# Optimization experiments

Hardware: AMD Instinct MI355X
Metric: run time of the kernel (lower is better)

## Reference

```python
import math
import jax, jax.numpy as jnp
import numpy as np

NUM_HEADS = 16
N_WIRES = 8  # d_k, fixed by the quantum circuit
EMBED_DIM = NUM_HEADS * N_WIRES  # 128
BATCH = 4
SEQ = 2048


def setup_inputs() -> dict:
    key = jax.random.key(0)
    k1, k2, k3, k4 = jax.random.split(key, 4)
    x = jax.random.normal(k1, (BATCH, SEQ, EMBED_DIM), dtype=jnp.float32)
    theta = jax.random.normal(k2, (N_WIRES,), dtype=jnp.float32)
    Wc = jax.random.normal(k3, (EMBED_DIM, EMBED_DIM), dtype=jnp.float32) / math.sqrt(EMBED_DIM)
    bc = jax.random.normal(k4, (EMBED_DIM,), dtype=jnp.float32) * 0.01
    return {"x": x, "theta": theta, "Wc": Wc, "bc": bc}


def reference(x, theta, Wc, bc):
    # x: (B, S, E). Quantum layer: per (token, head), RX-encode the 8-dim slice,
    # apply trainable RX, measure PauliZ -> cos(x_i + theta_i) per wire (product state).
    B, S, E = x.shape
    H, dk = NUM_HEADS, N_WIRES
    proj = jnp.cos(x.reshape(B, S, H, dk) + theta)          # (B, S, H, dk)
    q = proj.transpose(0, 2, 1, 3)                          # (B, H, S, dk); q == k == v
    scale = 1.0 / math.sqrt(dk)
    scores = jnp.einsum('bhqd,bhkd->bhqk', q, q) * scale    # (B, H, S, S)
    attn = jax.nn.softmax(scores, axis=-1)                  # dropout p=0 (eval)
    out = jnp.einsum('bhqk,bhkd->bhqd', attn, q)            # (B, H, S, dk)
    merged = out.transpose(0, 2, 1, 3).reshape(B, S, E)     # (B, S, E)
    return merged @ Wc.T + bc                               # combine_heads Linear
```

## Files before the change

### kernel.cpp

```cpp
#include <hip/hip_runtime.h>
#include <math.h>

#define B_  4
#define S_  2048
#define H_  16
#define DK_ 8
#define E_  128

typedef _Float16 f16x8  __attribute__((ext_vector_type(8)));
typedef __fp16   h2     __attribute__((ext_vector_type(2)));
typedef float    f32x16 __attribute__((ext_vector_type(16)));
typedef int      i32x2  __attribute__((ext_vector_type(2)));

union U4  { unsigned u[4]; f16x8 v; uint4 q; };
union H2U { h2 h; unsigned u; };

#define KSC 0.51006972f

static __device__ __forceinline__ float fexp2(float x) {
#if __has_builtin(__builtin_amdgcn_exp2f)
    return __builtin_amdgcn_exp2f(x);
#else
    return __builtin_exp2f(x);
#endif
}

static __device__ __forceinline__ float frcp(float x) {
#if __has_builtin(__builtin_amdgcn_rcpf)
    return __builtin_amdgcn_rcpf(x);
#else
    return 1.0f / x;
#endif
}

__global__ __launch_bounds__(1024, 8)
void qattn_mfma(const float* __restrict__ x, const float* __restrict__ theta,
                float* __restrict__ out) {
    constexpr int VST = 2056;
    __shared__ __align__(16) _Float16 smem[S_ * DK_ + 9 * VST];
    _Float16* Klds = smem;
    _Float16* Vt   = smem + S_ * DK_;

    const int tid  = threadIdx.x;
    const int lane = tid & 63;
    const int wv   = tid >> 6;
    const int bh   = blockIdx.y;
    const int b    = bh >> 4;
    const int h    = bh & 15;

    {
        float th[DK_];
#pragma unroll
        for (int d = 0; d < DK_; ++d) th[d] = theta[d];

        const float* xp = x + ((size_t)b * S_) * E_ + h * DK_;
        const int s0 = tid * 2;
        float4 a0 = *(const float4*)(xp + (size_t)s0 * E_);
        float4 a1 = *(const float4*)(xp + (size_t)s0 * E_ + 4);
        float4 b0 = *(const float4*)(xp + (size_t)(s0 + 1) * E_);
        float4 b1 = *(const float4*)(xp + (size_t)(s0 + 1) * E_ + 4);
        float ca[8], cb[8];
        ca[0]=__cosf(a0.x+th[0]); ca[1]=__cosf(a0.y+th[1]); ca[2]=__cosf(a0.z+th[2]); ca[3]=__cosf(a0.w+th[3]);
        ca[4]=__cosf(a1.x+th[4]); ca[5]=__cosf(a1.y+th[5]); ca[6]=__cosf(a1.z+th[6]); ca[7]=__cosf(a1.w+th[7]);
        cb[0]=__cosf(b0.x+th[0]); cb[1]=__cosf(b0.y+th[1]); cb[2]=__cosf(b0.z+th[2]); cb[3]=__cosf(b0.w+th[3]);
        cb[4]=__cosf(b1.x+th[4]); cb[5]=__cosf(b1.y+th[5]); cb[6]=__cosf(b1.z+th[6]); cb[7]=__cosf(b1.w+th[7]);

        H2U p0, p1, p2, p3;
        p0.h = __builtin_amdgcn_cvt_pkrtz(ca[0], ca[1]);
        p1.h = __builtin_amdgcn_cvt_pkrtz(ca[2], ca[3]);
        p2.h = __builtin_amdgcn_cvt_pkrtz(ca[4], ca[5]);
        p3.h = __builtin_amdgcn_cvt_pkrtz(ca[6], ca[7]);
        *(uint4*)&Klds[(size_t)s0 * DK_] = make_uint4(p0.u, p1.u, p2.u, p3.u);
        p0.h = __builtin_amdgcn_cvt_pkrtz(cb[0], cb[1]);
        p1.h = __builtin_amdgcn_cvt_pkrtz(cb[2], cb[3]);
        p2.h = __builtin_amdgcn_cvt_pkrtz(cb[4], cb[5]);
        p3.h = __builtin_amdgcn_cvt_pkrtz(cb[6], cb[7]);
        *(uint4*)&Klds[(size_t)(s0 + 1) * DK_] = make_uint4(p0.u, p1.u, p2.u, p3.u);

#pragma unroll
        for (int d = 0; d < DK_; ++d) {
            H2U tv; tv.h = __builtin_amdgcn_cvt_pkrtz(ca[d], cb[d]);
            *(unsigned*)&Vt[d * VST + s0] = tv.u;
        }
        *(unsigned*)&Vt[8 * VST + s0] = 0x3C003C00u;
    }
    __syncthreads();

    const int  qg    = wv & 7;
    const int  kh    = wv >> 3;
    const int  qrow0 = blockIdx.x * 256 + qg * 32;
    const int  t0    = kh * 32;
    const int  l31   = lane & 31;
    const int  hi    = lane >> 5;
    const bool lo32  = (lane < 32);

    f16x8 qf = {};
    if (lo32) {
        qf = *(const f16x8*)&Klds[(size_t)(qrow0 + l31) * DK_];
#pragma unroll
        for (int d = 0; d < DK_; ++d)
            qf[d] = qf[d] * (_Float16)KSC;
    }

    const f32x16 z16 = {};
    f32x16 accO = {};

    const int nc = (l31 <= 8) ? l31 : 8;
    const _Float16* vbase = &Vt[nc * VST + hi * 8];

    for (int kt = t0; kt < t0 + 32; ++kt) {
        f16x8 kf = *(const f16x8*)&Klds[(size_t)(kt * 32 + l31) * DK_];
        f32x16 sc = __builtin_amdgcn_mfma_f32_32x32x16_f16(kf, qf, z16, 0, 0, 0);

        unsigned X[4][2];
#pragma unroll
        for (int q = 0; q < 4; ++q) {
            float w0 = fexp2(sc[4 * q + 0]);
            float w1 = fexp2(sc[4 * q + 1]);
            float w2 = fexp2(sc[4 * q + 2]);
            float w3 = fexp2(sc[4 * q + 3]);
            H2U p0, p1;
            p0.h = __builtin_amdgcn_cvt_pkrtz(w0, w1);
            p1.h = __builtin_amdgcn_cvt_pkrtz(w2, w3);
            X[q][0] = p0.u; X[q][1] = p1.u;
        }

#pragma unroll
        for (int s = 0; s < 2; ++s) {
            U4 pa;
#pragma unroll
            for (int i = 0; i < 2; ++i) {
                i32x2 r = __builtin_amdgcn_permlane32_swap(
                    (int)X[2 * s][i], (int)X[2 * s + 1][i], false, false);
                pa.u[i]     = (unsigned)r[0];
                pa.u[2 + i] = (unsigned)r[1];
            }
            f16x8 vf = *(const f16x8*)(vbase + kt * 32 + s * 16);
            accO = __builtin_amdgcn_mfma_f32_32x32x16_f16(pa.v, vf, accO, 0, 0, 0);
        }
    }

    __syncthreads();
    float* scratch = (float*)smem;
    if (kh == 1) {
        float4* dst = (float4*)&scratch[(size_t)(qg * 64 + lane) * 16];
#pragma unroll
        for (int i = 0; i < 4; ++i)
            dst[i] = make_float4(accO[4*i], accO[4*i+1], accO[4*i+2], accO[4*i+3]);
    }
    __syncthreads();
    if (kh == 0) {
        const float4* src = (const float4*)&scratch[(size_t)(qg * 64 + lane) * 16];
#pragma unroll
        for (int i = 0; i < 4; ++i) {
            float4 p = src[i];
            accO[4*i+0] += p.x; accO[4*i+1] += p.y;
            accO[4*i+2] += p.z; accO[4*i+3] += p.w;
        }

        const int n = l31;
        float* obase = out + ((size_t)(b * S_ + qrow0)) * E_ + h * DK_ + n;
#pragma unroll
        for (int i = 0; i < 16; ++i) {
            float den = __shfl(accO[i], (lane & 32) | 8, 64);
            float val = accO[i] * frcp(den);
            int row = (i & 3) + 8 * (i >> 2) + 4 * hi;
            if (n < DK_) obase[(size_t)row * E_] = val;
        }
    }
}

__global__ __launch_bounds__(256, 2)
void proj_mfma(const float* __restrict__ Wc, const float* __restrict__ bc,
               float* __restrict__ io) {
    __shared__ __align__(16) _Float16 As[64 * E_];
    __shared__ __align__(16) _Float16 Bs[E_ * E_];
    const int tid  = threadIdx.x;
    const int lane = tid & 63;
    const int wv   = tid >> 6;
    const int l31  = lane & 31;
    const int hi   = lane >> 5;
    const int r0   = blockIdx.x * 64;

    for (int i = tid; i < 64 * 16; i += 256) {
        int r = i >> 4, c = i & 15;
        const float* s = io + (size_t)(r0 + r) * E_ + c * 8;
        float4 a = *(const float4*)s;
        float4 b = *(const float4*)(s + 4);
        H2U p0, p1, p2, p3;
        p0.h = __builtin_amdgcn_cvt_pkrtz(a.x, a.y);
        p1.h = __builtin_amdgcn_cvt_pkrtz(a.z, a.w);
        p2.h = __builtin_amdgcn_cvt_pkrtz(b.x, b.y);
        p3.h = __builtin_amdgcn_cvt_pkrtz(b.z, b.w);
        *(uint4*)&As[r * E_ + ((c ^ (r & 7)) * 8)] = make_uint4(p0.u, p1.u, p2.u, p3.u);
    }
    for (int i = tid; i < E_ * 16; i += 256) {
        int r = i >> 4, c = i & 15;
        const float* s = Wc + (size_t)r * E_ + c * 8;
        float4 a = *(const float4*)s;
        float4 b = *(const float4*)(s + 4);
        H2U p0, p1, p2, p3;
        p0.h = __builtin_amdgcn_cvt_pkrtz(a.x, a.y);
        p1.h = __builtin_amdgcn_cvt_pkrtz(a.z, a.w);
        p2.h = __builtin_amdgcn_cvt_pkrtz(b.x, b.y);
        p3.h = __builtin_amdgcn_cvt_pkrtz(b.z, b.w);
        *(uint4*)&Bs[r * E_ + ((c ^ (r & 7)) * 8)] = make_uint4(p0.u, p1.u, p2.u, p3.u);
    }
    __syncthreads();

    const int rg = wv & 1;
    const int cp = (wv >> 1) * 2;

    f32x16 acc0 = {}, acc1 = {};
#pragma unroll
    for (int ks = 0; ks < 8; ++ks) {
        int ch = (ks * 2 + hi);
        f16x8 af  = *(const f16x8*)&As[(rg * 32 + l31) * E_ + ((ch ^ (l31 & 7)) * 8)];
        f16x8 bf0 = *(const f16x8*)&Bs[((cp + 0) * 32 + l31) * E_ + ((ch ^ (l31 & 7)) * 8)];
        f16x8 bf1 = *(const f16x8*)&Bs[((cp + 1) * 32 + l31) * E_ + ((ch ^ (l31 & 7)) * 8)];
        acc0 = __builtin_amdgcn_mfma_f32_32x32x16_f16(af, bf0, acc0, 0, 0, 0);
        acc1 = __builtin_amdgcn_mfma_f32_32x32x16_f16(af, bf1, acc1, 0, 0, 0);
    }

    const float b0 = bc[(cp + 0) * 32 + l31];
    const float b1 = bc[(cp + 1) * 32 + l31];
#pragma unroll
    for (int i = 0; i < 16; ++i) {
        int row = (i & 3) + 8 * (i >> 2) + 4 * hi;
        float* orow = io + (size_t)(r0 + rg * 32 + row) * E_;
        orow[(cp + 0) * 32 + l31] = acc0[i] + b0;
        orow[(cp + 1) * 32 + l31] = acc1[i] + b1;
    }
}

extern "C" void kernel_launch(void* const* d_in, const int* in_sizes, int n_in,
                              void* d_out, int out_size, void* d_ws, size_t ws_size,
                              hipStream_t stream) {
    const float* x     = (const float*)d_in[0];
    const float* theta = (const float*)d_in[1];
    const float* Wc    = (const float*)d_in[2];
    const float* bc    = (const float*)d_in[3];
    float* out = (float*)d_out;

    qattn_mfma<<<dim3(S_ / 256, B_ * H_), 1024, 0, stream>>>(x, theta, out);
    proj_mfma<<<dim3((B_ * S_) / 64), 256, 0, stream>>>(Wc, bc, out);
}
```

Baseline: 47.93 us.

## Process two query tiles per wave to reuse K/V loads, stagger key order

Each wave now handles 64 query rows (two 32-row MFMA tiles) instead of 32, sharing each K fragment and V fragment load across both tiles, and the grid halves in x. The key-tile loop is rotated per wave to spread LDS bank accesses across waves. This halves the per-block K/V prologue (cos computation and LDS fill) relative to query work and halves LDS reads per query. The cost is higher register pressure, a lowered occupancy hint, and only 256 blocks, which may underfill the GPU.

```diff
diff --git a/kernel.cpp b/kernel.cpp
--- a/kernel.cpp
+++ b/kernel.cpp
@@ -33,7 +33,7 @@
 #endif
 }
 
-__global__ __launch_bounds__(1024, 8)
+__global__ __launch_bounds__(1024, 4)
 void qattn_mfma(const float* __restrict__ x, const float* __restrict__ theta,
                 float* __restrict__ out) {
     constexpr int VST = 2056;
@@ -88,85 +88,113 @@
 
     const int  qg    = wv & 7;
     const int  kh    = wv >> 3;
-    const int  qrow0 = blockIdx.x * 256 + qg * 32;
+    const int  qrow0 = blockIdx.x * 512 + qg * 64;
     const int  t0    = kh * 32;
+    const int  rot   = (wv * 2) & 31;
     const int  l31   = lane & 31;
     const int  hi    = lane >> 5;
     const bool lo32  = (lane < 32);
 
-    f16x8 qf = {};
+    f16x8 qf0 = {}, qf1 = {};
     if (lo32) {
-        qf = *(const f16x8*)&Klds[(size_t)(qrow0 + l31) * DK_];
-#pragma unroll
-        for (int d = 0; d < DK_; ++d)
-            qf[d] = qf[d] * (_Float16)KSC;
+        qf0 = *(const f16x8*)&Klds[(size_t)(qrow0 + l31) * DK_];
+        qf1 = *(const f16x8*)&Klds[(size_t)(qrow0 + 32 + l31) * DK_];
+#pragma unroll
+        for (int d = 0; d < DK_; ++d) {
+            qf0[d] = qf0[d] * (_Float16)KSC;
+            qf1[d] = qf1[d] * (_Float16)KSC;
+        }
     }
 
     const f32x16 z16 = {};
-    f32x16 accO = {};
+    f32x16 accO0 = {}, accO1 = {};
 
     const int nc = (l31 <= 8) ? l31 : 8;
     const _Float16* vbase = &Vt[nc * VST + hi * 8];
 
-    for (int kt = t0; kt < t0 + 32; ++kt) {
+    for (int i = 0; i < 32; ++i) {
+        const int kt = t0 + ((i + rot) & 31);
         f16x8 kf = *(const f16x8*)&Klds[(size_t)(kt * 32 + l31) * DK_];
-        f32x16 sc = __builtin_amdgcn_mfma_f32_32x32x16_f16(kf, qf, z16, 0, 0, 0);
-
-        unsigned X[4][2];
+        f32x16 sc0 = __builtin_amdgcn_mfma_f32_32x32x16_f16(kf, qf0, z16, 0, 0, 0);
+        f32x16 sc1 = __builtin_amdgcn_mfma_f32_32x32x16_f16(kf, qf1, z16, 0, 0, 0);
+
+        unsigned X0[4][2], X1[4][2];
 #pragma unroll
         for (int q = 0; q < 4; ++q) {
-            float w0 = fexp2(sc[4 * q + 0]);
-            float w1 = fexp2(sc[4 * q + 1]);
-            float w2 = fexp2(sc[4 * q + 2]);
-            float w3 = fexp2(sc[4 * q + 3]);
-            H2U p0, p1;
-            p0.h = __builtin_amdgcn_cvt_pkrtz(w0, w1);
-            p1.h = __builtin_amdgcn_cvt_pkrtz(w2, w3);
-            X[q][0] = p0.u; X[q][1] = p1.u;
+            float a0 = fexp2(sc0[4*q+0]), a1 = fexp2(sc0[4*q+1]);
+            float a2 = fexp2(sc0[4*q+2]), a3 = fexp2(sc0[4*q+3]);
+            float b0 = fexp2(sc1[4*q+0]), b1 = fexp2(sc1[4*q+1]);
+            float b2 = fexp2(sc1[4*q+2]), b3 = fexp2(sc1[4*q+3]);
+            H2U u0, u1, u2, u3;
+            u0.h = __builtin_amdgcn_cvt_pkrtz(a0, a1);
+            u1.h = __builtin_amdgcn_cvt_pkrtz(a2, a3);
+            u2.h = __builtin_amdgcn_cvt_pkrtz(b0, b1);
+            u3.h = __builtin_amdgcn_cvt_pkrtz(b2, b3);
+            X0[q][0] = u0.u; X0[q][1] = u1.u;
+            X1[q][0] = u2.u; X1[q][1] = u3.u;
         }
 
 #pragma unroll
         for (int s = 0; s < 2; ++s) {
-            U4 pa;
-#pragma unroll
-            for (int i = 0; i < 2; ++i) {
-                i32x2 r = __builtin_amdgcn_permlane32_swap(
-                    (int)X[2 * s][i], (int)X[2 * s + 1][i], false, false);
-                pa.u[i]     = (unsigned)r[0];
-                pa.u[2 + i] = (unsigned)r[1];
+            f16x8 vf = *(const f16x8*)(vbase + kt * 32 + s * 16);
+            U4 pa0, pa1;
+#pragma unroll
+            for (int j = 0; j < 2; ++j) {
+                i32x2 r0 = __builtin_amdgcn_permlane32_swap(
+                    (int)X0[2*s][j], (int)X0[2*s+1][j], false, false);
+                pa0.u[j]     = (unsigned)r0[0];
+                pa0.u[2 + j] = (unsigned)r0[1];
+                i32x2 r1 = __builtin_amdgcn_permlane32_swap(
+                    (int)X1[2*s][j], (int)X1[2*s+1][j], false, false);
+                pa1.u[j]     = (unsigned)r1[0];
+                pa1.u[2 + j] = (unsigned)r1[1];
             }
-            f16x8 vf = *(const f16x8*)(vbase + kt * 32 + s * 16);
-            accO = __builtin_amdgcn_mfma_f32_32x32x16_f16(pa.v, vf, accO, 0, 0, 0);
+            accO0 = __builtin_amdgcn_mfma_f32_32x32x16_f16(pa0.v, vf, accO0, 0, 0, 0);
+            accO1 = __builtin_amdgcn_mfma_f32_32x32x16_f16(pa1.v, vf, accO1, 0, 0, 0);
         }
     }
 
     __syncthreads();
     float* scratch = (float*)smem;
     if (kh == 1) {
-        float4* dst = (float4*)&scratch[(size_t)(qg * 64 + lane) * 16];
-#pragma unroll
-        for (int i = 0; i < 4; ++i)
-            dst[i] = make_float4(accO[4*i], accO[4*i+1], accO[4*i+2], accO[4*i+3]);
+        float4* d0 = (float4*)&scratch[(size_t)((qg * 2 + 0) * 64 + lane) * 16];
+        float4* d1 = (float4*)&scratch[(size_t)((qg * 2 + 1) * 64 + lane) * 16];
+#pragma unroll
+        for (int i = 0; i < 4; ++i) {
+            d0[i] = make_float4(accO0[4*i], accO0[4*i+1], accO0[4*i+2], accO0[4*i+3]);
+            d1[i] = make_float4(accO1[4*i], accO1[4*i+1], accO1[4*i+2], accO1[4*i+3]);
+        }
     }
     __syncthreads();
     if (kh == 0) {
-        const float4* src = (const float4*)&scratch[(size_t)(qg * 64 + lane) * 16];
+        const float4* s0 = (const float4*)&scratch[(size_t)((qg * 2 + 0) * 64 + lane) * 16];
+        const float4* s1 = (const float4*)&scratch[(size_t)((qg * 2 + 1) * 64 + lane) * 16];
 #pragma unroll
         for (int i = 0; i < 4; ++i) {
-            float4 p = src[i];
-            accO[4*i+0] += p.x; accO[4*i+1] += p.y;
-            accO[4*i+2] += p.z; accO[4*i+3] += p.w;
+            float4 p = s0[i];
+            accO0[4*i+0] += p.x; accO0[4*i+1] += p.y;
+            accO0[4*i+2] += p.z; accO0[4*i+3] += p.w;
+            float4 q = s1[i];
+            accO1[4*i+0] += q.x; accO1[4*i+1] += q.y;
+            accO1[4*i+2] += q.z; accO1[4*i+3] += q.w;
         }
 
         const int n = l31;
-        float* obase = out + ((size_t)(b * S_ + qrow0)) * E_ + h * DK_ + n;
-#pragma unroll
-        for (int i = 0; i < 16; ++i) {
-            float den = __shfl(accO[i], (lane & 32) | 8, 64);
-            float val = accO[i] * frcp(den);
-            int row = (i & 3) + 8 * (i >> 2) + 4 * hi;
-            if (n < DK_) obase[(size_t)row * E_] = val;
-        }
+#define EPILOG(ACC, C)                                                          \
+        {                                                                       \
+            float* obase = out + ((size_t)(b * S_ + qrow0 + (C) * 32)) * E_     \
+                         + h * DK_ + n;                                         \
+            _Pragma("unroll")                                                   \
+            for (int i = 0; i < 16; ++i) {                                      \
+                float den = __shfl(ACC[i], (lane & 32) | 8, 64);                \
+                float val = ACC[i] * frcp(den);                                 \
+                int row = (i & 3) + 8 * (i >> 2) + 4 * hi;                      \
+                if (n < DK_) obase[(size_t)row * E_] = val;                     \
+            }                                                                   \
+        }
+        EPILOG(accO0, 0)
+        EPILOG(accO1, 1)
+#undef EPILOG
     }
 }
 
@@ -242,6 +270,6 @@
     const float* bc    = (const float*)d_in[3];
     float* out = (float*)d_out;
 
-    qattn_mfma<<<dim3(S_ / 256, B_ * H_), 1024, 0, stream>>>(x, theta, out);
+    qattn_mfma<<<dim3(S_ / 512, B_ * H_), 1024, 0, stream>>>(x, theta, out);
     proj_mfma<<<dim3((B_ * S_) / 64), 256, 0, stream>>>(Wc, bc, out);
 }
```

After: 49.20 us. +2.6%, slower.
